# Kernel optimization log

Hardware: AMD Instinct MI355X
Metric: run time of the kernel (lower is better)

Reference implementation:

```python
import jax, jax.numpy as jnp
import numpy as np
import math

B, C, L, N, HEAD, M, DEPTH = 16, 256, 64, 8192, 8, 12, 1
PI = math.pi
MODES = jnp.arange(M, dtype=jnp.float32) / M  # modes_list = i/num_basis


def conv1d(x, w, b=None):
    # 1x1 Conv1d == channel matmul. x: (B,Cin,T), w: (Cout,Cin)
    y = jnp.einsum('oc,bcn->bon', w, x)
    if b is not None:
        y = y + b[None, :, None]
    return y


def split_heads(x):
    # (B,C,T) -> (B,H,T,c)  matching view(B,head,C//head,T).permute(0,1,3,2)
    b, c, t = x.shape
    return x.reshape(b, HEAD, c // HEAD, t).transpose(0, 1, 3, 2)


def merge_heads(x):
    # (B,H,T,c) -> (B,C,T)
    b, h, t, c = x.shape
    return x.transpose(0, 1, 3, 2).reshape(b, h * c, t)


def self_attn(q, k, v):
    # NOTE: source multiplies by dim**0.5 (not 1/sqrt(dim)); keep faithful.
    dim = q.shape[-1]
    a = jax.nn.softmax(jnp.einsum('bhlc,bhsc->bhls', q, k) * (dim ** 0.5), axis=-1)
    return jnp.einsum('bhls,bhsc->bhlc', a, v)


def encoder(x, enc_w, enc_b, weights):
    b, c, l = x.shape
    qkv = conv1d(x, enc_w, enc_b).reshape(b, 3, c, l)
    q = split_heads(qkv[:, 0])
    k = split_heads(qkv[:, 1])
    v = split_heads(qkv[:, 2])
    attn = merge_heads(self_attn(q, k, v))  # (B,C,L)
    # Fourier basis: cat(sin, cos) over num_basis modes -> (B,C,L,2M)
    ph = MODES[None, None, None, :] * attn[..., None] * PI
    basis = jnp.concatenate([jnp.sin(ph), jnp.cos(ph)], axis=-1)
    return jnp.einsum('bclm,cm->bcl', basis, weights) + x


def decoder(x, attn, dec_w, dec_b):
    kv = split_heads(attn)                      # (B,H,L,c) latent keys/values
    q = split_heads(conv1d(x, dec_w, dec_b))    # (B,H,N,c) point queries
    return merge_heads(self_attn(q, kv, kv)) + x


def bn_lrelu(x, g, b):
    # eval-mode BatchNorm1d (running_mean=0, running_var=1, eps=1e-5) + LeakyReLU(0.2)
    y = g[None, :, None] * x / jnp.sqrt(1.0 + 1e-5) + b[None, :, None]
    return jnp.where(y >= 0, y, 0.2 * y)


def setup_inputs() -> dict:
    key = jax.random.key(0)
    ks = jax.random.split(key, 8)
    return {
        'xt': jax.random.normal(ks[0], (B, C, L), jnp.float32),
        'xn': jax.random.normal(ks[1], (B, C, N), jnp.float32),
        'weights': jax.random.uniform(ks[2], (C, 2 * M), jnp.float32) / C,
        'mask_token': jax.random.normal(ks[3], (1, C, 1), jnp.float32) * 0.02,
        'enc_w': jax.random.normal(ks[4], (3 * C, C), jnp.float32) * 0.02,
        'enc_b': jnp.zeros((3 * C,), jnp.float32),
        'dec_w': jax.random.normal(ks[5], (C, C), jnp.float32) * 0.02,
        'dec_b': jnp.zeros((C,), jnp.float32),
        'fc1_w': jax.random.normal(ks[6], (C, C), jnp.float32) * 0.02,
        'fc1_g': jnp.ones((C,), jnp.float32),
        'fc1_b': jnp.zeros((C,), jnp.float32),
        'fc2_w': jax.random.normal(ks[7], (3, C), jnp.float32) * 0.02,
        'fc2_g': jnp.ones((3,), jnp.float32),
        'fc2_b': jnp.zeros((3,), jnp.float32),
    }


def reference(xt, xn, weights, mask_token, enc_w, enc_b, dec_w, dec_b,
              fc1_w, fc1_g, fc1_b, fc2_w, fc2_g, fc2_b):
    b = xt.shape[0]
    n = xn.shape[-1]
    # ratio=1.0 -> len_keep=0 -> fully masked: mask_token broadcast, under no_grad
    x_masked = jax.lax.stop_gradient(jnp.broadcast_to(mask_token, (b, C, n)))
    enc = xt
    x = x_masked
    for _ in range(DEPTH):
        enc = encoder(enc, enc_w, enc_b, weights)
        x = decoder(x, enc, dec_w, dec_b)
    xn_pre = x
    y = bn_lrelu(conv1d(xn_pre, fc1_w), fc1_g, fc1_b)
    y = bn_lrelu(conv1d(y, fc2_w), fc2_g, fc2_b)  # (B,3,N)
    return xn_pre, y.transpose(0, 2, 1)  # ((B,C,N), (B,N,3))
```

## Files before the change

### kernel.cpp

```cpp
#include <hip/hip_runtime.h>
#include <hip/hip_bf16.h>
#include <math.h>

#define B_    16
#define C_    256
#define L_    64
#define N_    8192
#define HEAD_ 8
#define HC_   32
#define M_    12

#define SQRT32F 5.656854249492380f
#define PI_F    3.14159265358979323846f
#define BN_INV  0.99999500003749969f

typedef float v4f __attribute__((ext_vector_type(4)));

__global__ __launch_bounds__(512) void fused_enc(
    const float* __restrict__ xt, const float* __restrict__ enc_w,
    const float* __restrict__ enc_b, const float* __restrict__ weights,
    const float* __restrict__ dec_w, const float* __restrict__ dec_b,
    const float* __restrict__ mt, float* __restrict__ xnp_out)
{
    __shared__ float Xs[C_][L_];
    __shared__ float qkv_s[96][68];
    __shared__ float P[L_][68];
    __shared__ float enc_t[HC_][68];
    __shared__ float wts[HC_][24];
    __shared__ float qvs[HC_];
    __shared__ float aw[L_];
    const int t = threadIdx.x;
    const int b = blockIdx.x >> 3;
    const int h = blockIdx.x & 7;
    const float* xtb = xt + (size_t)b * (C_ * L_);

    #pragma unroll
    for (int i = 0; i < 8; ++i) {
        int q = t + i * 512;
        int c = q >> 4, l4 = (q & 15) * 4;
        *reinterpret_cast<float4*>(&Xs[c][l4]) =
            *reinterpret_cast<const float4*>(&xtb[q * 4]);
    }
    #pragma unroll
    for (int idx = t; idx < HC_ * 24; idx += 512)
        wts[idx / 24][idx % 24] = weights[(h * HC_) * 24 + idx];
    __syncthreads();

    {
        const int tx = t & 15, ty = t >> 4;
        float acc[3][4] = {};
        int og[3];
        const float* wrow[3];
        #pragma unroll
        for (int r = 0; r < 3; ++r) {
            int o_loc = ty * 3 + r;
            int sec = o_loc >> 5, cc = o_loc & 31;
            og[r] = sec * C_ + h * HC_ + cc;
            wrow[r] = enc_w + (size_t)og[r] * C_;
        }
        #pragma unroll 2
        for (int c0 = 0; c0 < C_; c0 += 4) {
            float4 x0 = *reinterpret_cast<const float4*>(&Xs[c0 + 0][tx * 4]);
            float4 x1 = *reinterpret_cast<const float4*>(&Xs[c0 + 1][tx * 4]);
            float4 x2 = *reinterpret_cast<const float4*>(&Xs[c0 + 2][tx * 4]);
            float4 x3 = *reinterpret_cast<const float4*>(&Xs[c0 + 3][tx * 4]);
            #pragma unroll
            for (int r = 0; r < 3; ++r) {
                float4 w4 = *reinterpret_cast<const float4*>(&wrow[r][c0]);
                acc[r][0] += w4.x * x0.x + w4.y * x1.x + w4.z * x2.x + w4.w * x3.x;
                acc[r][1] += w4.x * x0.y + w4.y * x1.y + w4.z * x2.y + w4.w * x3.y;
                acc[r][2] += w4.x * x0.z + w4.y * x1.z + w4.z * x2.z + w4.w * x3.z;
                acc[r][3] += w4.x * x0.w + w4.y * x1.w + w4.z * x2.w + w4.w * x3.w;
            }
        }
        #pragma unroll
        for (int r = 0; r < 3; ++r) {
            float bias = enc_b[og[r]];
            float4 v = make_float4(acc[r][0] + bias, acc[r][1] + bias,
                                   acc[r][2] + bias, acc[r][3] + bias);
            *reinterpret_cast<float4*>(&qkv_s[ty * 3 + r][tx * 4]) = v;
        }
    }
    if (t < 128) {
        int cc = t >> 2, part = t & 3;
        const float* wr = dec_w + (size_t)(h * HC_ + cc) * C_ + part * 64;
        const float* mp = mt + part * 64;
        float s = 0.f;
        #pragma unroll
        for (int j = 0; j < 16; ++j) {
            float4 w4 = *reinterpret_cast<const float4*>(&wr[j * 4]);
            float4 m4 = *reinterpret_cast<const float4*>(&mp[j * 4]);
            s += w4.x * m4.x + w4.y * m4.y + w4.z * m4.z + w4.w * m4.w;
        }
        s += __shfl_xor(s, 1);
        s += __shfl_xor(s, 2);
        if (part == 0) qvs[cc] = s + dec_b[h * HC_ + cc];
    }
    __syncthreads();

    {
        const int l0  = (t >> 4) * 2;
        const int lp0 = (t & 15) * 4;
        float sc[2][4] = {};
        #pragma unroll
        for (int cc = 0; cc < HC_; ++cc) {
            float2 q2 = *reinterpret_cast<const float2*>(&qkv_s[cc][l0]);
            float4 k4 = *reinterpret_cast<const float4*>(&qkv_s[32 + cc][lp0]);
            sc[0][0] += q2.x * k4.x; sc[0][1] += q2.x * k4.y;
            sc[0][2] += q2.x * k4.z; sc[0][3] += q2.x * k4.w;
            sc[1][0] += q2.y * k4.x; sc[1][1] += q2.y * k4.y;
            sc[1][2] += q2.y * k4.z; sc[1][3] += q2.y * k4.w;
        }
        #pragma unroll
        for (int i = 0; i < 2; ++i) {
            float4 v = make_float4(sc[i][0] * SQRT32F, sc[i][1] * SQRT32F,
                                   sc[i][2] * SQRT32F, sc[i][3] * SQRT32F);
            *reinterpret_cast<float4*>(&P[l0 + i][lp0]) = v;
        }
    }
    __syncthreads();

    {
        int l = t >> 3, p0 = (t & 7) * 8;
        float m = -1e30f;
        #pragma unroll
        for (int j = 0; j < 8; ++j) m = fmaxf(m, P[l][p0 + j]);
        m = fmaxf(m, __shfl_xor(m, 1));
        m = fmaxf(m, __shfl_xor(m, 2));
        m = fmaxf(m, __shfl_xor(m, 4));
        float sum = 0.f;
        #pragma unroll
        for (int j = 0; j < 8; ++j) {
            float e = __expf(P[l][p0 + j] - m);
            P[l][p0 + j] = e;
            sum += e;
        }
        sum += __shfl_xor(sum, 1);
        sum += __shfl_xor(sum, 2);
        sum += __shfl_xor(sum, 4);
        float inv = 1.0f / sum;
        #pragma unroll
        for (int j = 0; j < 8; ++j) P[l][p0 + j] *= inv;
    }
    __syncthreads();

    {
        const int l0 = (t & 31) * 2;
        const int c0 = (t >> 5) * 2;
        float a[2][2] = {};
        #pragma unroll
        for (int sq = 0; sq < 16; ++sq) {
            float4 p0v = *reinterpret_cast<const float4*>(&P[l0 + 0][sq * 4]);
            float4 p1v = *reinterpret_cast<const float4*>(&P[l0 + 1][sq * 4]);
            float4 v0v = *reinterpret_cast<const float4*>(&qkv_s[64 + c0 + 0][sq * 4]);
            float4 v1v = *reinterpret_cast<const float4*>(&qkv_s[64 + c0 + 1][sq * 4]);
            a[0][0] += p0v.x * v0v.x + p0v.y * v0v.y + p0v.z * v0v.z + p0v.w * v0v.w;
            a[0][1] += p0v.x * v1v.x + p0v.y * v1v.y + p0v.z * v1v.z + p0v.w * v1v.w;
            a[1][0] += p1v.x * v0v.x + p1v.y * v0v.y + p1v.z * v0v.z + p1v.w * v0v.w;
            a[1][1] += p1v.x * v1v.x + p1v.y * v1v.y + p1v.z * v1v.z + p1v.w * v1v.w;
        }
        #pragma unroll
        for (int j = 0; j < 2; ++j) {
            int cc = c0 + j;
            int c  = h * HC_ + cc;
            const float* wrf = wts[cc];
            float vv[2];
            #pragma unroll
            for (int i = 0; i < 2; ++i) {
                float val = Xs[c][l0 + i] + wrf[M_];
                float base = a[i][j] * (PI_F / (float)M_);
                float s1, c1;
                __sincosf(base, &s1, &c1);
                float sm = 0.f, cm = 1.f;
                #pragma unroll
                for (int m = 1; m < M_; ++m) {
                    float sp = sm * c1 + cm * s1;
                    float cp = cm * c1 - sm * s1;
                    sm = sp; cm = cp;
                    val += wrf[m] * sm + wrf[M_ + m] * cm;
                }
                vv[i] = val;
            }
            *reinterpret_cast<float2*>(&enc_t[cc][l0]) =
                make_float2(vv[0], vv[1]);
        }
    }
    __syncthreads();

    if (t < L_) {
        float s = 0.f;
        #pragma unroll
        for (int cc = 0; cc < HC_; ++cc) s += qvs[cc] * enc_t[cc][t];
        s *= SQRT32F;
        float m = s;
        #pragma unroll
        for (int off = 32; off >= 1; off >>= 1) m = fmaxf(m, __shfl_xor(m, off));
        float e = __expf(s - m);
        float sum = e;
        #pragma unroll
        for (int off = 32; off >= 1; off >>= 1) sum += __shfl_xor(sum, off);
        aw[t] = e / sum;
    }
    __syncthreads();
    if (t < HC_) {
        float a = 0.f;
        #pragma unroll
        for (int k4 = 0; k4 < L_; k4 += 4) {
            float4 a4 = *reinterpret_cast<const float4*>(&aw[k4]);
            float4 v4 = *reinterpret_cast<const float4*>(&enc_t[t][k4]);
            a += a4.x * v4.x + a4.y * v4.y + a4.z * v4.z + a4.w * v4.w;
        }
        int c = h * HC_ + t;
        xnp_out[b * C_ + c] = a + mt[c];
    }
}

__global__ __launch_bounds__(256) void bcast_fc(const float* __restrict__ xnp,
                                                const float* __restrict__ fc1_w,
                                                const float* __restrict__ fc1_g,
                                                const float* __restrict__ fc1_b,
                                                const float* __restrict__ fc2_w,
                                                const float* __restrict__ fc2_g,
                                                const float* __restrict__ fc2_b,
                                                float* __restrict__ out) {
    const int t = threadIdx.x;
    const int blk = blockIdx.x;
    if (blk >= 16) {
        int rowid = blk - 16;
        float v = xnp[rowid];
        v4f V = {v, v, v, v};
        v4f* row = reinterpret_cast<v4f*>(out + (size_t)rowid * N_);
        #pragma unroll
        for (int i = 0; i < 8; ++i)
            __builtin_nontemporal_store(V, &row[t + i * 256]);
    } else {
        int b = blk;
        __shared__ float xs[C_];
        __shared__ float y1[C_];
        __shared__ float y2s[4];
        xs[t] = xnp[b * C_ + t];
        __syncthreads();
        {
            const float* wrow = fc1_w + (size_t)t * C_;
            float s = 0.f;
            #pragma unroll 8
            for (int c4 = 0; c4 < C_; c4 += 4) {
                float4 w4 = *reinterpret_cast<const float4*>(&wrow[c4]);
                float4 x4 = *reinterpret_cast<const float4*>(&xs[c4]);
                s += w4.x * x4.x + w4.y * x4.y + w4.z * x4.z + w4.w * x4.w;
            }
            float y = fc1_g[t] * s * BN_INV + fc1_b[t];
            y1[t] = (y >= 0.f) ? y : 0.2f * y;
        }
        __syncthreads();
        if (t < 3) {
            const float* wrow = fc2_w + t * C_;
            float s = 0.f;
            #pragma unroll 8
            for (int c4 = 0; c4 < C_; c4 += 4) {
                float4 w4 = *reinterpret_cast<const float4*>(&wrow[c4]);
                float4 x4 = *reinterpret_cast<const float4*>(&y1[c4]);
                s += w4.x * x4.x + w4.y * x4.y + w4.z * x4.z + w4.w * x4.w;
            }
            float y = fc2_g[t] * s * BN_INV + fc2_b[t];
            y2s[t] = (y >= 0.f) ? y : 0.2f * y;
        }
        __syncthreads();
        float v0 = y2s[0], v1 = y2s[1], v2 = y2s[2];
        v4f pat0 = {v0, v1, v2, v0};
        v4f pat1 = {v1, v2, v0, v1};
        v4f pat2 = {v2, v0, v1, v2};
        int r = t % 3;
        v4f a = (r == 0) ? pat0 : (r == 1) ? pat1 : pat2;
        v4f bb = (r == 0) ? pat1 : (r == 1) ? pat2 : pat0;
        v4f c = (r == 0) ? pat2 : (r == 1) ? pat0 : pat1;
        v4f* o1 = reinterpret_cast<v4f*>(
            out + (size_t)B_ * C_ * N_ + (size_t)b * (N_ * 3));
        #pragma unroll
        for (int i = 0; i < 24; i += 3) {
            __builtin_nontemporal_store(a,  &o1[t + (i + 0) * 256]);
            __builtin_nontemporal_store(bb, &o1[t + (i + 1) * 256]);
            __builtin_nontemporal_store(c,  &o1[t + (i + 2) * 256]);
        }
    }
}

extern "C" void kernel_launch(void* const* d_in, const int* in_sizes, int n_in,
                              void* d_out, int out_size, void* d_ws, size_t ws_size,
                              hipStream_t stream) {
    const float* xt      = (const float*)d_in[0];
    const float* weights = (const float*)d_in[2];
    const float* mt      = (const float*)d_in[3];
    const float* enc_w   = (const float*)d_in[4];
    const float* enc_b   = (const float*)d_in[5];
    const float* dec_w   = (const float*)d_in[6];
    const float* dec_b   = (const float*)d_in[7];
    const float* fc1_w   = (const float*)d_in[8];
    const float* fc1_g   = (const float*)d_in[9];
    const float* fc1_b   = (const float*)d_in[10];
    const float* fc2_w   = (const float*)d_in[11];
    const float* fc2_g   = (const float*)d_in[12];
    const float* fc2_b   = (const float*)d_in[13];

    float* ws  = (float*)d_ws;
    float* xnp = ws;

    float* out = (float*)d_out;

    fused_enc<<<128, 512, 0, stream>>>(xt, enc_w, enc_b, weights,
                                       dec_w, dec_b, mt, xnp);
    bcast_fc<<<4112, 256, 0, stream>>>(xnp, fc1_w, fc1_g, fc1_b,
                                       fc2_w, fc2_g, fc2_b, out);
}
```

Before: 52.41 us.

## Split QKV projection into separate tiled GEMM kernel before attention

Moves the encoder QKV 1x1-conv projection out of the fused per-(batch,head) kernel into a standalone shared-memory tiled GEMM across 384 blocks. The mask-token decoder query projection is also computed once there, instead of redundantly in every block. The attention kernel then reads its QKV slice and a small xt slice from global workspace. The aim is more parallelism than the 128-block fused kernel, at the cost of an extra launch and a global round trip of the QKV intermediate.

New measurement: 54.79 us. 4.5% more time.

```diff
diff --git a/kernel.cpp b/kernel.cpp
--- a/kernel.cpp
+++ b/kernel.cpp
@@ -9,6 +9,7 @@
 #define HEAD_ 8
 #define HC_   32
 #define M_    12
+#define BL_   1024
 
 #define SQRT32F 5.656854249492380f
 #define PI_F    3.14159265358979323846f
@@ -16,86 +17,124 @@
 
 typedef float v4f __attribute__((ext_vector_type(4)));
 
-__global__ __launch_bounds__(512) void fused_enc(
-    const float* __restrict__ xt, const float* __restrict__ enc_w,
-    const float* __restrict__ enc_b, const float* __restrict__ weights,
-    const float* __restrict__ dec_w, const float* __restrict__ dec_b,
+__global__ __launch_bounds__(128) void qkv_gemm(const float* __restrict__ enc_w,
+                                                const float* __restrict__ enc_b,
+                                                const float* __restrict__ xt,
+                                                const float* __restrict__ dec_w,
+                                                const float* __restrict__ dec_b,
+                                                const float* __restrict__ mt,
+                                                float* __restrict__ Y,
+                                                float* __restrict__ qv_out) {
+    __shared__ float As_t[32][36];
+    __shared__ float Bs[32][64];
+    const int t = threadIdx.x;
+
+    if (blockIdx.y == 24) {
+        if (blockIdx.x != 0) return;
+        __shared__ float mts[C_];
+        mts[t] = mt[t];
+        mts[t + 128] = mt[t + 128];
+        __syncthreads();
+        #pragma unroll
+        for (int rr = 0; rr < 2; ++rr) {
+            int r = t + rr * 128;
+            const float* wrow = dec_w + (size_t)r * C_;
+            float s = 0.f;
+            #pragma unroll 8
+            for (int c4 = 0; c4 < C_; c4 += 4) {
+                float4 w4 = *reinterpret_cast<const float4*>(&wrow[c4]);
+                float4 m4 = *reinterpret_cast<const float4*>(&mts[c4]);
+                s += w4.x * m4.x + w4.y * m4.y + w4.z * m4.z + w4.w * m4.w;
+            }
+            qv_out[r] = s + dec_b[r];
+        }
+        return;
+    }
+
+    const int b  = blockIdx.x;
+    const int o0 = blockIdx.y * 32;
+    const float* xb = xt + (size_t)b * (C_ * L_);
+    const int tx = t & 15;
+    const int ty = t >> 4;
+    float4 acc[4] = {};
+
+    for (int k0 = 0; k0 < 256; k0 += 32) {
+        #pragma unroll
+        for (int i = 0; i < 2; ++i) {
+            int q = t + i * 128;
+            int kk4 = (q & 7) * 4, r = q >> 3;
+            float4 w4 = *reinterpret_cast<const float4*>(
+                &enc_w[(size_t)(o0 + r) * 256 + k0 + kk4]);
+            As_t[kk4 + 0][r] = w4.x;
+            As_t[kk4 + 1][r] = w4.y;
+            As_t[kk4 + 2][r] = w4.z;
+            As_t[kk4 + 3][r] = w4.w;
+        }
+        #pragma unroll
+        for (int i = 0; i < 4; ++i) {
+            int q = t + i * 128;
+            int jj4 = (q & 15) * 4, kk = q >> 4;
+            *reinterpret_cast<float4*>(&Bs[kk][jj4]) =
+                *reinterpret_cast<const float4*>(&xb[(k0 + kk) * 64 + jj4]);
+        }
+        __syncthreads();
+        #pragma unroll
+        for (int kk = 0; kk < 32; ++kk) {
+            float4 a4 = *reinterpret_cast<const float4*>(&As_t[kk][ty * 4]);
+            float4 b4 = *reinterpret_cast<const float4*>(&Bs[kk][tx * 4]);
+            float as[4] = {a4.x, a4.y, a4.z, a4.w};
+            #pragma unroll
+            for (int ii = 0; ii < 4; ++ii) {
+                acc[ii].x += as[ii] * b4.x; acc[ii].y += as[ii] * b4.y;
+                acc[ii].z += as[ii] * b4.z; acc[ii].w += as[ii] * b4.w;
+            }
+        }
+        __syncthreads();
+    }
+    #pragma unroll
+    for (int ii = 0; ii < 4; ++ii) {
+        int o = o0 + ty * 4 + ii;
+        float bias = enc_b[o];
+        float4 w = acc[ii];
+        w.x += bias; w.y += bias; w.z += bias; w.w += bias;
+        *reinterpret_cast<float4*>(&Y[(size_t)o * BL_ + b * 64 + tx * 4]) = w;
+    }
+}
+
+__global__ __launch_bounds__(512) void attn_dec(
+    const float* __restrict__ Y, const float* __restrict__ xt,
+    const float* __restrict__ weights, const float* __restrict__ qv_in,
     const float* __restrict__ mt, float* __restrict__ xnp_out)
 {
-    __shared__ float Xs[C_][L_];
     __shared__ float qkv_s[96][68];
     __shared__ float P[L_][68];
     __shared__ float enc_t[HC_][68];
+    __shared__ float xts[HC_][68];
     __shared__ float wts[HC_][24];
     __shared__ float qvs[HC_];
     __shared__ float aw[L_];
     const int t = threadIdx.x;
     const int b = blockIdx.x >> 3;
     const int h = blockIdx.x & 7;
-    const float* xtb = xt + (size_t)b * (C_ * L_);
 
     #pragma unroll
-    for (int i = 0; i < 8; ++i) {
-        int q = t + i * 512;
-        int c = q >> 4, l4 = (q & 15) * 4;
-        *reinterpret_cast<float4*>(&Xs[c][l4]) =
-            *reinterpret_cast<const float4*>(&xtb[q * 4]);
+    for (int i = 0; i < 3; ++i) {
+        int idx = t + i * 512;
+        int row = idx >> 4, q4 = (idx & 15) * 4;
+        int o = (row >> 5) * C_ + h * HC_ + (row & 31);
+        *reinterpret_cast<float4*>(&qkv_s[row][q4]) =
+            *reinterpret_cast<const float4*>(&Y[(size_t)o * BL_ + b * 64 + q4]);
+    }
+    {
+        int cc = t >> 4, q4 = (t & 15) * 4;
+        *reinterpret_cast<float4*>(&xts[cc][q4]) =
+            *reinterpret_cast<const float4*>(
+                &xt[((size_t)b * C_ + h * HC_ + cc) * L_ + q4]);
     }
     #pragma unroll
     for (int idx = t; idx < HC_ * 24; idx += 512)
         wts[idx / 24][idx % 24] = weights[(h * HC_) * 24 + idx];
-    __syncthreads();
-
-    {
-        const int tx = t & 15, ty = t >> 4;
-        float acc[3][4] = {};
-        int og[3];
-        const float* wrow[3];
-        #pragma unroll
-        for (int r = 0; r < 3; ++r) {
-            int o_loc = ty * 3 + r;
-            int sec = o_loc >> 5, cc = o_loc & 31;
-            og[r] = sec * C_ + h * HC_ + cc;
-            wrow[r] = enc_w + (size_t)og[r] * C_;
-        }
-        #pragma unroll 2
-        for (int c0 = 0; c0 < C_; c0 += 4) {
-            float4 x0 = *reinterpret_cast<const float4*>(&Xs[c0 + 0][tx * 4]);
-            float4 x1 = *reinterpret_cast<const float4*>(&Xs[c0 + 1][tx * 4]);
-            float4 x2 = *reinterpret_cast<const float4*>(&Xs[c0 + 2][tx * 4]);
-            float4 x3 = *reinterpret_cast<const float4*>(&Xs[c0 + 3][tx * 4]);
-            #pragma unroll
-            for (int r = 0; r < 3; ++r) {
-                float4 w4 = *reinterpret_cast<const float4*>(&wrow[r][c0]);
-                acc[r][0] += w4.x * x0.x + w4.y * x1.x + w4.z * x2.x + w4.w * x3.x;
-                acc[r][1] += w4.x * x0.y + w4.y * x1.y + w4.z * x2.y + w4.w * x3.y;
-                acc[r][2] += w4.x * x0.z + w4.y * x1.z + w4.z * x2.z + w4.w * x3.z;
-                acc[r][3] += w4.x * x0.w + w4.y * x1.w + w4.z * x2.w + w4.w * x3.w;
-            }
-        }
-        #pragma unroll
-        for (int r = 0; r < 3; ++r) {
-            float bias = enc_b[og[r]];
-            float4 v = make_float4(acc[r][0] + bias, acc[r][1] + bias,
-                                   acc[r][2] + bias, acc[r][3] + bias);
-            *reinterpret_cast<float4*>(&qkv_s[ty * 3 + r][tx * 4]) = v;
-        }
-    }
-    if (t < 128) {
-        int cc = t >> 2, part = t & 3;
-        const float* wr = dec_w + (size_t)(h * HC_ + cc) * C_ + part * 64;
-        const float* mp = mt + part * 64;
-        float s = 0.f;
-        #pragma unroll
-        for (int j = 0; j < 16; ++j) {
-            float4 w4 = *reinterpret_cast<const float4*>(&wr[j * 4]);
-            float4 m4 = *reinterpret_cast<const float4*>(&mp[j * 4]);
-            s += w4.x * m4.x + w4.y * m4.y + w4.z * m4.z + w4.w * m4.w;
-        }
-        s += __shfl_xor(s, 1);
-        s += __shfl_xor(s, 2);
-        if (part == 0) qvs[cc] = s + dec_b[h * HC_ + cc];
-    }
+    if (t < HC_) qvs[t] = qv_in[h * HC_ + t];
     __syncthreads();
 
     {
@@ -162,12 +201,11 @@
         #pragma unroll
         for (int j = 0; j < 2; ++j) {
             int cc = c0 + j;
-            int c  = h * HC_ + cc;
             const float* wrf = wts[cc];
             float vv[2];
             #pragma unroll
             for (int i = 0; i < 2; ++i) {
-                float val = Xs[c][l0 + i] + wrf[M_];
+                float val = xts[cc][l0 + i] + wrf[M_];
                 float base = a[i][j] * (PI_F / (float)M_);
                 float s1, c1;
                 __sincosf(base, &s1, &c1);
@@ -303,12 +341,15 @@
     const float* fc2_b   = (const float*)d_in[13];
 
     float* ws  = (float*)d_ws;
-    float* xnp = ws;
+    float* Y   = ws;
+    float* qv  = ws + 786432;
+    float* xnp = ws + 786688;
 
     float* out = (float*)d_out;
 
-    fused_enc<<<128, 512, 0, stream>>>(xt, enc_w, enc_b, weights,
-                                       dec_w, dec_b, mt, xnp);
+    qkv_gemm<<<dim3(16, 25), 128, 0, stream>>>(enc_w, enc_b, xt,
+                                               dec_w, dec_b, mt, Y, qv);
+    attn_dec<<<128, 512, 0, stream>>>(Y, xt, weights, qv, mt, xnp);
     bcast_fc<<<4112, 256, 0, stream>>>(xnp, fc1_w, fc1_g, fc1_b,
                                        fc2_w, fc2_g, fc2_b, out);
 }
```

## Split encoder across query halves and move decoder attention to separate kernel

Applied to the files above, without the earlier changes.

The fused encoder kernel is split so each (batch, head) pair is handled by two blocks, each computing attention for half of the query positions. Each block still recomputes the full K and V but only half of Q. The encoder output goes to global memory, and a new small kernel performs the decoder's single-query attention. This doubles the grid from 128 to 256 blocks to fill more compute units, at the cost of duplicated K/V projection work, an extra kernel launch, and a global-memory round trip for the encoder output.

New measurement: 55.88 us. 6.6% more time.

```diff
diff --git a/kernel.cpp b/kernel.cpp
--- a/kernel.cpp
+++ b/kernel.cpp
@@ -16,22 +16,19 @@
 
 typedef float v4f __attribute__((ext_vector_type(4)));
 
-__global__ __launch_bounds__(512) void fused_enc(
+__global__ __launch_bounds__(512) void enc_half(
     const float* __restrict__ xt, const float* __restrict__ enc_w,
     const float* __restrict__ enc_b, const float* __restrict__ weights,
-    const float* __restrict__ dec_w, const float* __restrict__ dec_b,
-    const float* __restrict__ mt, float* __restrict__ xnp_out)
+    float* __restrict__ enc)
 {
     __shared__ float Xs[C_][L_];
     __shared__ float qkv_s[96][68];
-    __shared__ float P[L_][68];
-    __shared__ float enc_t[HC_][68];
+    __shared__ float P[32][68];
     __shared__ float wts[HC_][24];
-    __shared__ float qvs[HC_];
-    __shared__ float aw[L_];
-    const int t = threadIdx.x;
-    const int b = blockIdx.x >> 3;
-    const int h = blockIdx.x & 7;
+    const int t    = threadIdx.x;
+    const int b    = blockIdx.x >> 4;
+    const int h    = (blockIdx.x >> 1) & 7;
+    const int half = blockIdx.x & 1;
     const float* xtb = xt + (size_t)b * (C_ * L_);
 
     #pragma unroll
@@ -47,170 +44,190 @@
     __syncthreads();
 
     {
-        const int tx = t & 15, ty = t >> 4;
-        float acc[3][4] = {};
-        int og[3];
-        const float* wrow[3];
-        #pragma unroll
-        for (int r = 0; r < 3; ++r) {
-            int o_loc = ty * 3 + r;
-            int sec = o_loc >> 5, cc = o_loc & 31;
-            og[r] = sec * C_ + h * HC_ + cc;
-            wrow[r] = enc_w + (size_t)og[r] * C_;
-        }
+        const int kvr  = t >> 4;
+        const int kvc4 = (t & 15) * 4;
+        const int qr   = t >> 3;
+        const int qc4  = half * 32 + (t & 7) * 4;
+        const float* wk = enc_w + (size_t)(C_ + h * HC_ + kvr) * C_;
+        const float* wv = enc_w + (size_t)(2 * C_ + h * HC_ + kvr) * C_;
+        const float* wq = enc_w + (size_t)(h * HC_ + (qr & 31)) * C_;
+        float4 acck = {}, accv = {}, accq = {};
         #pragma unroll 2
         for (int c0 = 0; c0 < C_; c0 += 4) {
-            float4 x0 = *reinterpret_cast<const float4*>(&Xs[c0 + 0][tx * 4]);
-            float4 x1 = *reinterpret_cast<const float4*>(&Xs[c0 + 1][tx * 4]);
-            float4 x2 = *reinterpret_cast<const float4*>(&Xs[c0 + 2][tx * 4]);
-            float4 x3 = *reinterpret_cast<const float4*>(&Xs[c0 + 3][tx * 4]);
+            float4 xk0 = *reinterpret_cast<const float4*>(&Xs[c0 + 0][kvc4]);
+            float4 xk1 = *reinterpret_cast<const float4*>(&Xs[c0 + 1][kvc4]);
+            float4 xk2 = *reinterpret_cast<const float4*>(&Xs[c0 + 2][kvc4]);
+            float4 xk3 = *reinterpret_cast<const float4*>(&Xs[c0 + 3][kvc4]);
+            float4 wk4 = *reinterpret_cast<const float4*>(&wk[c0]);
+            float4 wv4 = *reinterpret_cast<const float4*>(&wv[c0]);
+            acck.x += wk4.x * xk0.x + wk4.y * xk1.x + wk4.z * xk2.x + wk4.w * xk3.x;
+            acck.y += wk4.x * xk0.y + wk4.y * xk1.y + wk4.z * xk2.y + wk4.w * xk3.y;
+            acck.z += wk4.x * xk0.z + wk4.y * xk1.z + wk4.z * xk2.z + wk4.w * xk3.z;
+            acck.w += wk4.x * xk0.w + wk4.y * xk1.w + wk4.z * xk2.w + wk4.w * xk3.w;
+            accv.x += wv4.x * xk0.x + wv4.y * xk1.x + wv4.z * xk2.x + wv4.w * xk3.x;
+            accv.y += wv4.x * xk0.y + wv4.y * xk1.y + wv4.z * xk2.y + wv4.w * xk3.y;
+            accv.z += wv4.x * xk0.z + wv4.y * xk1.z + wv4.z * xk2.z + wv4.w * xk3.z;
+            accv.w += wv4.x * xk0.w + wv4.y * xk1.w + wv4.z * xk2.w + wv4.w * xk3.w;
+            if (t < 256) {
+                float4 xq0 = *reinterpret_cast<const float4*>(&Xs[c0 + 0][qc4]);
+                float4 xq1 = *reinterpret_cast<const float4*>(&Xs[c0 + 1][qc4]);
+                float4 xq2 = *reinterpret_cast<const float4*>(&Xs[c0 + 2][qc4]);
+                float4 xq3 = *reinterpret_cast<const float4*>(&Xs[c0 + 3][qc4]);
+                float4 wq4 = *reinterpret_cast<const float4*>(&wq[c0]);
+                accq.x += wq4.x * xq0.x + wq4.y * xq1.x + wq4.z * xq2.x + wq4.w * xq3.x;
+                accq.y += wq4.x * xq0.y + wq4.y * xq1.y + wq4.z * xq2.y + wq4.w * xq3.y;
+                accq.z += wq4.x * xq0.z + wq4.y * xq1.z + wq4.z * xq2.z + wq4.w * xq3.z;
+                accq.w += wq4.x * xq0.w + wq4.y * xq1.w + wq4.z * xq2.w + wq4.w * xq3.w;
+            }
+        }
+        float bk = enc_b[C_ + h * HC_ + kvr];
+        float bv = enc_b[2 * C_ + h * HC_ + kvr];
+        acck.x += bk; acck.y += bk; acck.z += bk; acck.w += bk;
+        accv.x += bv; accv.y += bv; accv.z += bv; accv.w += bv;
+        *reinterpret_cast<float4*>(&qkv_s[32 + kvr][kvc4]) = acck;
+        *reinterpret_cast<float4*>(&qkv_s[64 + kvr][kvc4]) = accv;
+        if (t < 256) {
+            float bq = enc_b[h * HC_ + qr];
+            accq.x += bq; accq.y += bq; accq.z += bq; accq.w += bq;
+            *reinterpret_cast<float4*>(&qkv_s[qr][qc4]) = accq;
+        }
+    }
+    __syncthreads();
+
+    {
+        const int l   = t >> 4;
+        const int lp0 = (t & 15) * 4;
+        const int qcol = half * 32 + l;
+        float4 a4 = {0.f, 0.f, 0.f, 0.f};
+        #pragma unroll
+        for (int cc = 0; cc < HC_; ++cc) {
+            float qv_ = qkv_s[cc][qcol];
+            float4 k4 = *reinterpret_cast<const float4*>(&qkv_s[32 + cc][lp0]);
+            a4.x += qv_ * k4.x; a4.y += qv_ * k4.y;
+            a4.z += qv_ * k4.z; a4.w += qv_ * k4.w;
+        }
+        a4.x *= SQRT32F; a4.y *= SQRT32F; a4.z *= SQRT32F; a4.w *= SQRT32F;
+        *reinterpret_cast<float4*>(&P[l][lp0]) = a4;
+    }
+    __syncthreads();
+
+    {
+        int l = t >> 4, p0 = (t & 15) * 4;
+        float m = -1e30f;
+        #pragma unroll
+        for (int j = 0; j < 4; ++j) m = fmaxf(m, P[l][p0 + j]);
+        m = fmaxf(m, __shfl_xor(m, 1));
+        m = fmaxf(m, __shfl_xor(m, 2));
+        m = fmaxf(m, __shfl_xor(m, 4));
+        m = fmaxf(m, __shfl_xor(m, 8));
+        float sum = 0.f;
+        #pragma unroll
+        for (int j = 0; j < 4; ++j) {
+            float e = __expf(P[l][p0 + j] - m);
+            P[l][p0 + j] = e;
+            sum += e;
+        }
+        sum += __shfl_xor(sum, 1);
+        sum += __shfl_xor(sum, 2);
+        sum += __shfl_xor(sum, 4);
+        sum += __shfl_xor(sum, 8);
+        float inv = 1.0f / sum;
+        #pragma unroll
+        for (int j = 0; j < 4; ++j) P[l][p0 + j] *= inv;
+    }
+    __syncthreads();
+
+    {
+        const int l0 = (t & 15) * 2;
+        const int cc = t >> 4;
+        float a0 = 0.f, a1 = 0.f;
+        #pragma unroll
+        for (int sq = 0; sq < 16; ++sq) {
+            float4 p0v = *reinterpret_cast<const float4*>(&P[l0 + 0][sq * 4]);
+            float4 p1v = *reinterpret_cast<const float4*>(&P[l0 + 1][sq * 4]);
+            float4 v4  = *reinterpret_cast<const float4*>(&qkv_s[64 + cc][sq * 4]);
+            a0 += p0v.x * v4.x + p0v.y * v4.y + p0v.z * v4.z + p0v.w * v4.w;
+            a1 += p1v.x * v4.x + p1v.y * v4.y + p1v.z * v4.z + p1v.w * v4.w;
+        }
+        const float* wrf = wts[cc];
+        const int c  = h * HC_ + cc;
+        const int lg = half * 32 + l0;
+        float av[2] = {a0, a1};
+        float vv[2];
+        #pragma unroll
+        for (int i = 0; i < 2; ++i) {
+            float val = Xs[c][lg + i] + wrf[M_];
+            float base = av[i] * (PI_F / (float)M_);
+            float s1, c1;
+            __sincosf(base, &s1, &c1);
+            float sm = 0.f, cm = 1.f;
             #pragma unroll
-            for (int r = 0; r < 3; ++r) {
-                float4 w4 = *reinterpret_cast<const float4*>(&wrow[r][c0]);
-                acc[r][0] += w4.x * x0.x + w4.y * x1.x + w4.z * x2.x + w4.w * x3.x;
-                acc[r][1] += w4.x * x0.y + w4.y * x1.y + w4.z * x2.y + w4.w * x3.y;
-                acc[r][2] += w4.x * x0.z + w4.y * x1.z + w4.z * x2.z + w4.w * x3.z;
-                acc[r][3] += w4.x * x0.w + w4.y * x1.w + w4.z * x2.w + w4.w * x3.w;
+            for (int m = 1; m < M_; ++m) {
+                float sp = sm * c1 + cm * s1;
+                float cp = cm * c1 - sm * s1;
+                sm = sp; cm = cp;
+                val += wrf[m] * sm + wrf[M_ + m] * cm;
             }
-        }
-        #pragma unroll
-        for (int r = 0; r < 3; ++r) {
-            float bias = enc_b[og[r]];
-            float4 v = make_float4(acc[r][0] + bias, acc[r][1] + bias,
-                                   acc[r][2] + bias, acc[r][3] + bias);
-            *reinterpret_cast<float4*>(&qkv_s[ty * 3 + r][tx * 4]) = v;
-        }
-    }
-    if (t < 128) {
-        int cc = t >> 2, part = t & 3;
-        const float* wr = dec_w + (size_t)(h * HC_ + cc) * C_ + part * 64;
-        const float* mp = mt + part * 64;
+            vv[i] = val;
+        }
+        *reinterpret_cast<float2*>(&enc[((size_t)b * C_ + c) * L_ + lg]) =
+            make_float2(vv[0], vv[1]);
+    }
+}
+
+__global__ __launch_bounds__(64) void dec_attn(const float* __restrict__ enc,
+                                               const float* __restrict__ dec_w,
+                                               const float* __restrict__ dec_b,
+                                               const float* __restrict__ mt,
+                                               float* __restrict__ xnp_out) {
+    __shared__ float qvs[HC_];
+    __shared__ float aw[L_];
+    const int l = threadIdx.x;
+    const int b = blockIdx.x >> 3;
+    const int h = blockIdx.x & 7;
+    const float* ench = enc + ((size_t)b * C_ + h * HC_) * L_;
+
+    {
+        int r = l >> 1, part = l & 1;
+        const float* wr = dec_w + (size_t)(h * HC_ + r) * C_ + part * 128;
+        const float* mp = mt + part * 128;
         float s = 0.f;
         #pragma unroll
-        for (int j = 0; j < 16; ++j) {
+        for (int j = 0; j < 32; ++j) {
             float4 w4 = *reinterpret_cast<const float4*>(&wr[j * 4]);
             float4 m4 = *reinterpret_cast<const float4*>(&mp[j * 4]);
             s += w4.x * m4.x + w4.y * m4.y + w4.z * m4.z + w4.w * m4.w;
         }
         s += __shfl_xor(s, 1);
-        s += __shfl_xor(s, 2);
-        if (part == 0) qvs[cc] = s + dec_b[h * HC_ + cc];
-    }
-    __syncthreads();
-
-    {
-        const int l0  = (t >> 4) * 2;
-        const int lp0 = (t & 15) * 4;
-        float sc[2][4] = {};
-        #pragma unroll
-        for (int cc = 0; cc < HC_; ++cc) {
-            float2 q2 = *reinterpret_cast<const float2*>(&qkv_s[cc][l0]);
-            float4 k4 = *reinterpret_cast<const float4*>(&qkv_s[32 + cc][lp0]);
-            sc[0][0] += q2.x * k4.x; sc[0][1] += q2.x * k4.y;
-            sc[0][2] += q2.x * k4.z; sc[0][3] += q2.x * k4.w;
-            sc[1][0] += q2.y * k4.x; sc[1][1] += q2.y * k4.y;
-            sc[1][2] += q2.y * k4.z; sc[1][3] += q2.y * k4.w;
-        }
-        #pragma unroll
-        for (int i = 0; i < 2; ++i) {
-            float4 v = make_float4(sc[i][0] * SQRT32F, sc[i][1] * SQRT32F,
-                                   sc[i][2] * SQRT32F, sc[i][3] * SQRT32F);
-            *reinterpret_cast<float4*>(&P[l0 + i][lp0]) = v;
-        }
-    }
-    __syncthreads();
-
-    {
-        int l = t >> 3, p0 = (t & 7) * 8;
-        float m = -1e30f;
-        #pragma unroll
-        for (int j = 0; j < 8; ++j) m = fmaxf(m, P[l][p0 + j]);
-        m = fmaxf(m, __shfl_xor(m, 1));
-        m = fmaxf(m, __shfl_xor(m, 2));
-        m = fmaxf(m, __shfl_xor(m, 4));
-        float sum = 0.f;
-        #pragma unroll
-        for (int j = 0; j < 8; ++j) {
-            float e = __expf(P[l][p0 + j] - m);
-            P[l][p0 + j] = e;
-            sum += e;
-        }
-        sum += __shfl_xor(sum, 1);
-        sum += __shfl_xor(sum, 2);
-        sum += __shfl_xor(sum, 4);
-        float inv = 1.0f / sum;
-        #pragma unroll
-        for (int j = 0; j < 8; ++j) P[l][p0 + j] *= inv;
-    }
-    __syncthreads();
-
-    {
-        const int l0 = (t & 31) * 2;
-        const int c0 = (t >> 5) * 2;
-        float a[2][2] = {};
-        #pragma unroll
-        for (int sq = 0; sq < 16; ++sq) {
-            float4 p0v = *reinterpret_cast<const float4*>(&P[l0 + 0][sq * 4]);
-            float4 p1v = *reinterpret_cast<const float4*>(&P[l0 + 1][sq * 4]);
-            float4 v0v = *reinterpret_cast<const float4*>(&qkv_s[64 + c0 + 0][sq * 4]);
-            float4 v1v = *reinterpret_cast<const float4*>(&qkv_s[64 + c0 + 1][sq * 4]);
-            a[0][0] += p0v.x * v0v.x + p0v.y * v0v.y + p0v.z * v0v.z + p0v.w * v0v.w;
-            a[0][1] += p0v.x * v1v.x + p0v.y * v1v.y + p0v.z * v1v.z + p0v.w * v1v.w;
-            a[1][0] += p1v.x * v0v.x + p1v.y * v0v.y + p1v.z * v0v.z + p1v.w * v0v.w;
-            a[1][1] += p1v.x * v1v.x + p1v.y * v1v.y + p1v.z * v1v.z + p1v.w * v1v.w;
-        }
-        #pragma unroll
-        for (int j = 0; j < 2; ++j) {
-            int cc = c0 + j;
-            int c  = h * HC_ + cc;
-            const float* wrf = wts[cc];
-            float vv[2];
-            #pragma unroll
-            for (int i = 0; i < 2; ++i) {
-                float val = Xs[c][l0 + i] + wrf[M_];
-                float base = a[i][j] * (PI_F / (float)M_);
-                float s1, c1;
-                __sincosf(base, &s1, &c1);
-                float sm = 0.f, cm = 1.f;
-                #pragma unroll
-                for (int m = 1; m < M_; ++m) {
-                    float sp = sm * c1 + cm * s1;
-                    float cp = cm * c1 - sm * s1;
-                    sm = sp; cm = cp;
-                    val += wrf[m] * sm + wrf[M_ + m] * cm;
-                }
-                vv[i] = val;
-            }
-            *reinterpret_cast<float2*>(&enc_t[cc][l0]) =
-                make_float2(vv[0], vv[1]);
-        }
-    }
-    __syncthreads();
-
-    if (t < L_) {
-        float s = 0.f;
-        #pragma unroll
-        for (int cc = 0; cc < HC_; ++cc) s += qvs[cc] * enc_t[cc][t];
-        s *= SQRT32F;
-        float m = s;
-        #pragma unroll
-        for (int off = 32; off >= 1; off >>= 1) m = fmaxf(m, __shfl_xor(m, off));
-        float e = __expf(s - m);
-        float sum = e;
-        #pragma unroll
-        for (int off = 32; off >= 1; off >>= 1) sum += __shfl_xor(sum, off);
-        aw[t] = e / sum;
-    }
-    __syncthreads();
-    if (t < HC_) {
+        if (part == 0) qvs[r] = s + dec_b[h * HC_ + r];
+    }
+    __syncthreads();
+
+    float s = 0.f;
+    #pragma unroll
+    for (int cc = 0; cc < HC_; ++cc)
+        s += qvs[cc] * ench[cc * L_ + l];
+    s *= SQRT32F;
+    float m = s;
+    #pragma unroll
+    for (int off = 32; off >= 1; off >>= 1) m = fmaxf(m, __shfl_xor(m, off));
+    float e = __expf(s - m);
+    float sum = e;
+    #pragma unroll
+    for (int off = 32; off >= 1; off >>= 1) sum += __shfl_xor(sum, off);
+    aw[l] = e / sum;
+    __syncthreads();
+
+    if (l < HC_) {
+        const float* vrow = ench + l * L_;
         float a = 0.f;
         #pragma unroll
         for (int k4 = 0; k4 < L_; k4 += 4) {
             float4 a4 = *reinterpret_cast<const float4*>(&aw[k4]);
-            float4 v4 = *reinterpret_cast<const float4*>(&enc_t[t][k4]);
+            float4 v4 = *reinterpret_cast<const float4*>(&vrow[k4]);
             a += a4.x * v4.x + a4.y * v4.y + a4.z * v4.z + a4.w * v4.w;
         }
-        int c = h * HC_ + t;
+        int c = h * HC_ + l;
         xnp_out[b * C_ + c] = a + mt[c];
     }
 }
@@ -303,12 +320,13 @@
     const float* fc2_b   = (const float*)d_in[13];
 
     float* ws  = (float*)d_ws;
-    float* xnp = ws;
+    float* enc = ws;
+    float* xnp = ws + 262144;
 
     float* out = (float*)d_out;
 
-    fused_enc<<<128, 512, 0, stream>>>(xt, enc_w, enc_b, weights,
-                                       dec_w, dec_b, mt, xnp);
+    enc_half<<<256, 512, 0, stream>>>(xt, enc_w, enc_b, weights, enc);
+    dec_attn<<<128, 64, 0, stream>>>(enc, dec_w, dec_b, mt, xnp);
     bcast_fc<<<4112, 256, 0, stream>>>(xnp, fc1_w, fc1_g, fc1_b,
                                        fc2_w, fc2_g, fc2_b, out);
 }
```

## Fuse xn_pre broadcast store into encoder kernel, shrink FC kernel to sixteen blocks

Applied to the files above, without the earlier changes.

The 128 MB broadcast of xn_pre over N moves out of the second kernel's 4096 row blocks and into the tail of the fused encoder kernel. Each of its 128 blocks now writes its 32 channel rows right after computing them, keeping the values in shared memory. The second kernel keeps only the small FC head and the (B,N,3) output. This removes the global round-trip of xnp before the big store and most of the second launch, but the whole store now runs on only 128 blocks, so per-CU store throughput could limit it.

New measurement: 57.92 us. 1.1x slower.

```diff
diff --git a/kernel.cpp b/kernel.cpp
--- a/kernel.cpp
+++ b/kernel.cpp
@@ -20,7 +20,8 @@
     const float* __restrict__ xt, const float* __restrict__ enc_w,
     const float* __restrict__ enc_b, const float* __restrict__ weights,
     const float* __restrict__ dec_w, const float* __restrict__ dec_b,
-    const float* __restrict__ mt, float* __restrict__ xnp_out)
+    const float* __restrict__ mt, float* __restrict__ xnp_out,
+    float* __restrict__ out)
 {
     __shared__ float Xs[C_][L_];
     __shared__ float qkv_s[96][68];
@@ -29,6 +30,7 @@
     __shared__ float wts[HC_][24];
     __shared__ float qvs[HC_];
     __shared__ float aw[L_];
+    __shared__ float xnp_s[HC_];
     const int t = threadIdx.x;
     const int b = blockIdx.x >> 3;
     const int h = blockIdx.x & 7;
@@ -211,77 +213,82 @@
             a += a4.x * v4.x + a4.y * v4.y + a4.z * v4.z + a4.w * v4.w;
         }
         int c = h * HC_ + t;
-        xnp_out[b * C_ + c] = a + mt[c];
+        float x = a + mt[c];
+        xnp_s[t] = x;
+        xnp_out[b * C_ + c] = x;
+    }
+    __syncthreads();
+
+    {
+        float* base = out + ((size_t)b * C_ + h * HC_) * N_;
+        #pragma unroll 4
+        for (int r = 0; r < HC_; ++r) {
+            float v = xnp_s[r];
+            v4f V = {v, v, v, v};
+            v4f* rp = reinterpret_cast<v4f*>(base + (size_t)r * N_);
+            #pragma unroll
+            for (int i = 0; i < 4; ++i)
+                __builtin_nontemporal_store(V, &rp[t + i * 512]);
+        }
     }
 }
 
-__global__ __launch_bounds__(256) void bcast_fc(const float* __restrict__ xnp,
-                                                const float* __restrict__ fc1_w,
-                                                const float* __restrict__ fc1_g,
-                                                const float* __restrict__ fc1_b,
-                                                const float* __restrict__ fc2_w,
-                                                const float* __restrict__ fc2_g,
-                                                const float* __restrict__ fc2_b,
-                                                float* __restrict__ out) {
+__global__ __launch_bounds__(256) void fc_out1(const float* __restrict__ xnp,
+                                               const float* __restrict__ fc1_w,
+                                               const float* __restrict__ fc1_g,
+                                               const float* __restrict__ fc1_b,
+                                               const float* __restrict__ fc2_w,
+                                               const float* __restrict__ fc2_g,
+                                               const float* __restrict__ fc2_b,
+                                               float* __restrict__ out) {
     const int t = threadIdx.x;
-    const int blk = blockIdx.x;
-    if (blk >= 16) {
-        int rowid = blk - 16;
-        float v = xnp[rowid];
-        v4f V = {v, v, v, v};
-        v4f* row = reinterpret_cast<v4f*>(out + (size_t)rowid * N_);
-        #pragma unroll
-        for (int i = 0; i < 8; ++i)
-            __builtin_nontemporal_store(V, &row[t + i * 256]);
-    } else {
-        int b = blk;
-        __shared__ float xs[C_];
-        __shared__ float y1[C_];
-        __shared__ float y2s[4];
-        xs[t] = xnp[b * C_ + t];
-        __syncthreads();
-        {
-            const float* wrow = fc1_w + (size_t)t * C_;
-            float s = 0.f;
-            #pragma unroll 8
-            for (int c4 = 0; c4 < C_; c4 += 4) {
-                float4 w4 = *reinterpret_cast<const float4*>(&wrow[c4]);
-                float4 x4 = *reinterpret_cast<const float4*>(&xs[c4]);
-                s += w4.x * x4.x + w4.y * x4.y + w4.z * x4.z + w4.w * x4.w;
-            }
-            float y = fc1_g[t] * s * BN_INV + fc1_b[t];
-            y1[t] = (y >= 0.f) ? y : 0.2f * y;
-        }
-        __syncthreads();
-        if (t < 3) {
-            const float* wrow = fc2_w + t * C_;
-            float s = 0.f;
-            #pragma unroll 8
-            for (int c4 = 0; c4 < C_; c4 += 4) {
-                float4 w4 = *reinterpret_cast<const float4*>(&wrow[c4]);
-                float4 x4 = *reinterpret_cast<const float4*>(&y1[c4]);
-                s += w4.x * x4.x + w4.y * x4.y + w4.z * x4.z + w4.w * x4.w;
-            }
-            float y = fc2_g[t] * s * BN_INV + fc2_b[t];
-            y2s[t] = (y >= 0.f) ? y : 0.2f * y;
-        }
-        __syncthreads();
-        float v0 = y2s[0], v1 = y2s[1], v2 = y2s[2];
-        v4f pat0 = {v0, v1, v2, v0};
-        v4f pat1 = {v1, v2, v0, v1};
-        v4f pat2 = {v2, v0, v1, v2};
-        int r = t % 3;
-        v4f a = (r == 0) ? pat0 : (r == 1) ? pat1 : pat2;
-        v4f bb = (r == 0) ? pat1 : (r == 1) ? pat2 : pat0;
-        v4f c = (r == 0) ? pat2 : (r == 1) ? pat0 : pat1;
-        v4f* o1 = reinterpret_cast<v4f*>(
-            out + (size_t)B_ * C_ * N_ + (size_t)b * (N_ * 3));
-        #pragma unroll
-        for (int i = 0; i < 24; i += 3) {
-            __builtin_nontemporal_store(a,  &o1[t + (i + 0) * 256]);
-            __builtin_nontemporal_store(bb, &o1[t + (i + 1) * 256]);
-            __builtin_nontemporal_store(c,  &o1[t + (i + 2) * 256]);
-        }
+    const int b = blockIdx.x;
+    __shared__ float xs[C_];
+    __shared__ float y1[C_];
+    __shared__ float y2s[4];
+    xs[t] = xnp[b * C_ + t];
+    __syncthreads();
+    {
+        const float* wrow = fc1_w + (size_t)t * C_;
+        float s = 0.f;
+        #pragma unroll 8
+        for (int c4 = 0; c4 < C_; c4 += 4) {
+            float4 w4 = *reinterpret_cast<const float4*>(&wrow[c4]);
+            float4 x4 = *reinterpret_cast<const float4*>(&xs[c4]);
+            s += w4.x * x4.x + w4.y * x4.y + w4.z * x4.z + w4.w * x4.w;
+        }
+        float y = fc1_g[t] * s * BN_INV + fc1_b[t];
+        y1[t] = (y >= 0.f) ? y : 0.2f * y;
+    }
+    __syncthreads();
+    if (t < 3) {
+        const float* wrow = fc2_w + t * C_;
+        float s = 0.f;
+        #pragma unroll 8
+        for (int c4 = 0; c4 < C_; c4 += 4) {
+            float4 w4 = *reinterpret_cast<const float4*>(&wrow[c4]);
+            float4 x4 = *reinterpret_cast<const float4*>(&y1[c4]);
+            s += w4.x * x4.x + w4.y * x4.y + w4.z * x4.z + w4.w * x4.w;
+        }
+        float y = fc2_g[t] * s * BN_INV + fc2_b[t];
+        y2s[t] = (y >= 0.f) ? y : 0.2f * y;
+    }
+    __syncthreads();
+    float v0 = y2s[0], v1 = y2s[1], v2 = y2s[2];
+    v4f pat0 = {v0, v1, v2, v0};
+    v4f pat1 = {v1, v2, v0, v1};
+    v4f pat2 = {v2, v0, v1, v2};
+    int r = t % 3;
+    v4f a = (r == 0) ? pat0 : (r == 1) ? pat1 : pat2;
+    v4f bb = (r == 0) ? pat1 : (r == 1) ? pat2 : pat0;
+    v4f c = (r == 0) ? pat2 : (r == 1) ? pat0 : pat1;
+    v4f* o1 = reinterpret_cast<v4f*>(
+        out + (size_t)B_ * C_ * N_ + (size_t)b * (N_ * 3));
+    #pragma unroll
+    for (int i = 0; i < 24; i += 3) {
+        __builtin_nontemporal_store(a,  &o1[t + (i + 0) * 256]);
+        __builtin_nontemporal_store(bb, &o1[t + (i + 1) * 256]);
+        __builtin_nontemporal_store(c,  &o1[t + (i + 2) * 256]);
     }
 }
 
@@ -308,7 +315,7 @@
     float* out = (float*)d_out;
 
     fused_enc<<<128, 512, 0, stream>>>(xt, enc_w, enc_b, weights,
-                                       dec_w, dec_b, mt, xnp);
-    bcast_fc<<<4112, 256, 0, stream>>>(xnp, fc1_w, fc1_g, fc1_b,
-                                       fc2_w, fc2_g, fc2_b, out);
+                                       dec_w, dec_b, mt, xnp, out);
+    fc_out1<<<16, 256, 0, stream>>>(xnp, fc1_w, fc1_g, fc1_b,
+                                    fc2_w, fc2_g, fc2_b, out);
 }
```
